# Kernel optimization log

Measured on AMD Instinct MI355X. Metric: run time of the kernel, lower is better.

## Reference

```python
import jax, jax.numpy as jnp
import numpy as np

DIM = 2048
N_HEADS = 32
N_KV_HEADS = 8
HEAD_DIM = DIM // N_HEADS  # 64
MAX_SEQ_LEN = 2048
ROPE_THETA = 10000.0
ROPE_SCALE = 1.0  # ("linear", 1.0)


def build_rope_cache(seq_len):
    # standard half-rotation RoPE cache with linear position scaling
    inv_freq = 1.0 / (ROPE_THETA ** (jnp.arange(0, HEAD_DIM, 2, dtype=jnp.float32) / HEAD_DIM))
    t = jnp.arange(seq_len, dtype=jnp.float32) / ROPE_SCALE
    freqs = jnp.outer(t, inv_freq)                      # [S, HD/2]
    emb = jnp.concatenate([freqs, freqs], axis=-1)      # [S, HD]
    return jnp.cos(emb), jnp.sin(emb)


def apply_rope(x, cos, sin):
    # x: [B, S, H, D]; cos/sin: [S, D]
    c = cos[None, :, None, :]
    s = sin[None, :, None, :]
    x1, x2 = jnp.split(x, 2, axis=-1)
    rot = jnp.concatenate([-x2, x1], axis=-1)           # rotate_half
    return x * c + rot * s


def setup_inputs() -> dict:
    key = jax.random.key(0)
    kx, kq, kk, kv, ko = jax.random.split(key, 5)
    B, S = 1, 2048
    x = jax.random.normal(kx, (B, S, DIM), dtype=jnp.float32)
    # nn.Linear weights stored [out_features, in_features]
    wq = jax.random.normal(kq, (DIM, DIM), dtype=jnp.float32) * 0.02
    wk = jax.random.normal(kk, (HEAD_DIM * N_KV_HEADS, DIM), dtype=jnp.float32) * 0.02
    wv = jax.random.normal(kv, (HEAD_DIM * N_KV_HEADS, DIM), dtype=jnp.float32) * 0.02
    wo = jax.random.normal(ko, (DIM, DIM), dtype=jnp.float32) * 0.02
    return {"x": x, "wq": wq, "wk": wk, "wv": wv, "wo": wo}


def reference(x, wq, wk, wv, wo):
    B, S, _ = x.shape
    g = N_HEADS // N_KV_HEADS  # GQA expand factor
    q = (x @ wq.T).reshape(B, S, N_HEADS, HEAD_DIM)
    k = (x @ wk.T).reshape(B, S, N_KV_HEADS, HEAD_DIM)
    v = (x @ wv.T).reshape(B, S, N_KV_HEADS, HEAD_DIM)
    cos, sin = build_rope_cache(S)
    q = apply_rope(q, cos, sin)
    k = apply_rope(k, cos, sin)
    # group q heads with their kv head instead of repeat_interleave on k/v
    q = q.transpose(0, 2, 1, 3).reshape(B, N_KV_HEADS, g, S, HEAD_DIM)
    k = k.transpose(0, 2, 1, 3)   # [B, Hkv, S, D]
    v = v.transpose(0, 2, 1, 3)
    scale = 1.0 / jnp.sqrt(jnp.asarray(HEAD_DIM, dtype=x.dtype))
    scores = jnp.einsum('bhgqd,bhkd->bhgqk', q, k) * scale  # [B,Hkv,g,S,S]
    causal = jnp.tril(jnp.ones((S, S), dtype=bool))
    scores = jnp.where(causal[None, None, None, :, :], scores, -jnp.inf)
    p = jax.nn.softmax(scores, axis=-1)
    out = jnp.einsum('bhgqk,bhkd->bhgqd', p, v)             # [B,Hkv,g,S,D]
    out = out.reshape(B, N_HEADS, S, HEAD_DIM).transpose(0, 2, 1, 3).reshape(B, S, DIM)
    return out @ wo.T
```

## Files before the change

### kernel.cpp

```cpp
#include <hip/hip_runtime.h>
#include <hip/hip_bf16.h>
#include <cstdint>
#include <cstddef>

#define DIM_ 2048
#define SLEN 2048
#define NQH 32
#define NKVH 8
#define HDIM 64
#define KVDIM 512

typedef __attribute__((ext_vector_type(8))) short short8;
typedef __attribute__((ext_vector_type(4))) float f32x4;
typedef __attribute__((ext_vector_type(16))) float f32x16;
typedef __attribute__((ext_vector_type(4))) unsigned int u32x4;

#define QSCALE 0.1803368801111243f

__device__ __forceinline__ unsigned short f2bf(float f) {
  unsigned u = __builtin_bit_cast(unsigned, f);
  u += 0x7FFFu + ((u >> 16) & 1u);
  return (unsigned short)(u >> 16);
}

__device__ __forceinline__ unsigned cvt_pk_bf16(float lo, float hi) {
  unsigned r;
  asm("v_cvt_pk_bf16_f32 %0, %1, %2" : "=v"(r) : "v"(lo), "v"(hi));
  return r;
}

__device__ __forceinline__ void gload_lds16(const void* g, void* l) {
  __builtin_amdgcn_global_load_lds(
      (const __attribute__((address_space(1))) void*)g,
      (__attribute__((address_space(3))) void*)l, 16, 0, 0);
}

__global__ void cvt_bf16_kernel(const float* __restrict__ in,
                                unsigned short* __restrict__ out, int n) {
  int i = (blockIdx.x * blockDim.x + threadIdx.x) * 8;
  if (i >= n) return;
  float4 a = *(const float4*)(in + i);
  float4 b = *(const float4*)(in + i + 4);
  ushort4 o0, o1;
  o0.x = f2bf(a.x); o0.y = f2bf(a.y); o0.z = f2bf(a.z); o0.w = f2bf(a.w);
  o1.x = f2bf(b.x); o1.y = f2bf(b.y); o1.z = f2bf(b.z); o1.w = f2bf(b.w);
  *(ushort4*)(out + i) = o0;
  *(ushort4*)(out + i + 4) = o1;
}

__global__ void rope_table_kernel(float* __restrict__ cosT, float* __restrict__ sinT) {
  int idx = blockIdx.x * blockDim.x + threadIdx.x;
  int s = idx >> 5, i = idx & 31;
  float inv = expf(-(float)i * (9.210340371976184f / 32.0f));
  float fr = (float)s * inv;
  cosT[idx] = cosf(fr);
  sinT[idx] = sinf(fr);
}

#define GSTAGE(buf, kt)                                                        \
  do {                                                                         \
    _Pragma("unroll") for (int r = 0; r < 2; ++r) {                            \
      const int L = r * 512 + tid;                                             \
      const int row = L >> 3;                                                  \
      const int scb = ((L & 7) * 16) ^ ((row & 7) << 4);                       \
      gload_lds16((const char*)A + ((size_t)(row0 + row) * DIM_ + kt) * 2 + scb, \
                  sA[buf] + (size_t)(r * 512 + wv * 64) * 8);                  \
      gload_lds16((const char*)B + ((size_t)(col0 + row) * DIM_ + kt) * 2 + scb, \
                  sB[buf] + (size_t)(r * 512 + wv * 64) * 8);                  \
    }                                                                          \
  } while (0)

#define GCOMPUTE(cur)                                                          \
  do {                                                                         \
    _Pragma("unroll") for (int ks = 0; ks < 2; ++ks) {                         \
      short8 af[2], bfr[4];                                                    \
      _Pragma("unroll") for (int m = 0; m < 2; ++m) {                          \
        const int row = wr + m * 16 + lrow;                                    \
        const int cB = (ks * 64 + lkb) ^ ((row & 7) << 4);                     \
        af[m] = *(const short8*)(sA[cur] + row * 64 + (cB >> 1));              \
      }                                                                        \
      _Pragma("unroll") for (int n = 0; n < 4; ++n) {                          \
        const int row = wc + n * 16 + lrow;                                    \
        const int cB = (ks * 64 + lkb) ^ ((row & 7) << 4);                     \
        bfr[n] = *(const short8*)(sB[cur] + row * 64 + (cB >> 1));             \
      }                                                                        \
      _Pragma("unroll") for (int m = 0; m < 2; ++m)                            \
          _Pragma("unroll") for (int n = 0; n < 4; ++n) acc[m][n] =            \
              __builtin_amdgcn_mfma_f32_16x16x32_bf16(af[m], bfr[n],           \
                                                      acc[m][n], 0, 0, 0);     \
    }                                                                          \
  } while (0)

__global__ __launch_bounds__(512, 2)
void gemm_qkv(const unsigned short* __restrict__ A,
              const unsigned short* __restrict__ B,
              unsigned short* __restrict__ Qr,
              unsigned short* __restrict__ Kr,
              unsigned short* __restrict__ Vtp,
              const float* __restrict__ cosT,
              const float* __restrict__ sinT) {
  __shared__ unsigned short sA[2][128 * 64];
  __shared__ unsigned short sB[2][128 * 64];
  const int tid = threadIdx.x;
  const int wv = tid >> 6, ln = tid & 63;
  const int row0 = blockIdx.x * 128;
  const int col0 = blockIdx.y * 128;
  const int wr = (wv >> 1) * 32, wc = (wv & 1) * 64;
  const int lrow = ln & 15, lkb = (ln >> 4) * 16;
  f32x4 acc[2][4] = {};

  GSTAGE(0, 0);
  for (int t = 0; t < 32; ++t) {
    __syncthreads();
    if (t + 1 < 32) GSTAGE((t + 1) & 1, (t + 1) * 64);
    GCOMPUTE(t & 1);
  }
  const int orow = (ln >> 4) * 4;
  const int by = blockIdx.y;
  if (by < 16) {
#pragma unroll
    for (int m = 0; m < 2; ++m)
#pragma unroll
      for (int j = 0; j < 4; ++j) {
        const int s = row0 + wr + m * 16 + orow + j;
#pragma unroll
        for (int n = 0; n < 2; ++n) {
          const int d1 = n * 16 + lrow;
          const float cv = cosT[s * 32 + d1], sv = sinT[s * 32 + d1];
          const float x1 = acc[m][n][j], x2 = acc[m][n + 2][j];
          const size_t base = (size_t)s * DIM_ + col0 + wc + d1;
          Qr[base] = f2bf((x1 * cv - x2 * sv) * QSCALE);
          Qr[base + 32] = f2bf((x2 * cv + x1 * sv) * QSCALE);
        }
      }
  } else if (by < 20) {
    const int cb = col0 - 2048;
#pragma unroll
    for (int m = 0; m < 2; ++m)
#pragma unroll
      for (int j = 0; j < 4; ++j) {
        const int s = row0 + wr + m * 16 + orow + j;
#pragma unroll
        for (int n = 0; n < 2; ++n) {
          const int d1 = n * 16 + lrow;
          const float cv = cosT[s * 32 + d1], sv = sinT[s * 32 + d1];
          const float x1 = acc[m][n][j], x2 = acc[m][n + 2][j];
          const size_t base = (size_t)s * KVDIM + cb + wc + d1;
          Kr[base] = f2bf(x1 * cv - x2 * sv);
          Kr[base + 32] = f2bf(x2 * cv + x1 * sv);
        }
      }
  } else {
    const int cb = col0 - 2560;
#pragma unroll
    for (int m = 0; m < 2; ++m)
#pragma unroll
      for (int n = 0; n < 4; ++n)
#pragma unroll
        for (int j = 0; j < 4; ++j) {
          const int s = row0 + wr + m * 16 + orow + j;
          const int vc = cb + wc + n * 16 + lrow;
          Vtp[(size_t)vc * SLEN + s] = f2bf(acc[m][n][j]);
        }
  }
}

__global__ __launch_bounds__(512, 2)
void gemm_bt_f32(const unsigned short* __restrict__ A,
                 const unsigned short* __restrict__ B, float* __restrict__ C) {
  __shared__ unsigned short sA[2][128 * 64];
  __shared__ unsigned short sB[2][128 * 64];
  const int tid = threadIdx.x;
  const int wv = tid >> 6, ln = tid & 63;
  const int row0 = blockIdx.x * 128;
  const int col0 = blockIdx.y * 128;
  const int wr = (wv >> 1) * 32, wc = (wv & 1) * 64;
  const int lrow = ln & 15, lkb = (ln >> 4) * 16;
  f32x4 acc[2][4] = {};

  GSTAGE(0, 0);
  for (int t = 0; t < 32; ++t) {
    __syncthreads();
    if (t + 1 < 32) GSTAGE((t + 1) & 1, (t + 1) * 64);
    GCOMPUTE(t & 1);
  }
  const int orow = (ln >> 4) * 4;
#pragma unroll
  for (int m = 0; m < 2; ++m)
#pragma unroll
    for (int n = 0; n < 4; ++n)
#pragma unroll
      for (int j = 0; j < 4; ++j)
        C[(size_t)(row0 + wr + m * 16 + orow + j) * DIM_ + col0 + wc + n * 16 + lrow] =
            acc[m][n][j];
}

__global__ __launch_bounds__(256, 2)
void attn4_kernel(const unsigned short* __restrict__ Q,
                  const unsigned short* __restrict__ Kc,
                  const unsigned short* __restrict__ Vt,
                  unsigned short* __restrict__ AO) {
  __shared__ __align__(16) char smem[16384];
  const int id = blockIdx.x;
  const int kvh = id & 7, hg = (id >> 3) & 3;
  const int c = 15 - (id >> 5);
  const int h = kvh * 4 + hg;
  const int tid = threadIdx.x;
  const int w = tid >> 6, l = tid & 63;
  const int l31 = l & 31, hi = l >> 5;
  const int wq0 = c * 128 + w * 32;
  const int qrow = wq0 + l31;
  const int ntw = (wq0 + 95) >> 6;

  const unsigned short* Kb = Kc + kvh * HDIM;
  const unsigned short* Vb = Vt + (size_t)kvh * HDIM * SLEN;

  short8 qf[4];
  {
    const unsigned short* qp = Q + (size_t)qrow * DIM_ + h * HDIM + hi * 8;
#pragma unroll
    for (int d = 0; d < 4; ++d) qf[d] = *(const short8*)(qp + d * 16);
  }
  f32x16 o[2] = {};
  float mrun = -1e30f, lrun = 0.f;

  auto loadK = [&](short8* kf, int t) {
    const unsigned short* kp = Kb + (size_t)(t * 64 + l31) * KVDIM + hi * 8;
#pragma unroll
    for (int d = 0; d < 4; ++d) {
      kf[d] = *(const short8*)(kp + d * 16);
      kf[4 + d] = *(const short8*)(kp + 32 * KVDIM + d * 16);
    }
  };

  auto body = [&](int t, const short8* kf) {
    const int k0 = t * 64;
    short8 vf0[4], vf1[4];
    {
      const unsigned short* vp = Vb + (size_t)l31 * SLEN + k0 + hi * 8;
#pragma unroll
      for (int d = 0; d < 4; ++d) {
        vf0[d] = *(const short8*)(vp + d * 16);
        vf1[d] = *(const short8*)(vp + (size_t)32 * SLEN + d * 16);
      }
    }
    f32x16 s0 = {}, s1 = {};
    __builtin_amdgcn_s_setprio(1);
#pragma unroll
    for (int d = 0; d < 4; ++d) {
      s0 = __builtin_amdgcn_mfma_f32_32x32x16_bf16(kf[d], qf[d], s0, 0, 0, 0);
      s1 = __builtin_amdgcn_mfma_f32_32x32x16_bf16(kf[4 + d], qf[d], s1, 0, 0, 0);
    }
    __builtin_amdgcn_s_setprio(0);

    float p[32];
#pragma unroll
    for (int r = 0; r < 16; ++r) { p[r] = s0[r]; p[16 + r] = s1[r]; }
    if (k0 + 63 > wq0) {
#pragma unroll
      for (int r = 0; r < 16; ++r) {
        const int ka = k0 + (r & 3) + 8 * (r >> 2) + 4 * hi;
        if (ka > qrow) p[r] = -1e30f;
        if (ka + 32 > qrow) p[16 + r] = -1e30f;
      }
    }
    float t16[16];
#pragma unroll
    for (int i = 0; i < 16; ++i) t16[i] = fmaxf(p[i], p[i + 16]);
#pragma unroll
    for (int i = 0; i < 8; ++i) t16[i] = fmaxf(t16[i], t16[i + 8]);
#pragma unroll
    for (int i = 0; i < 4; ++i) t16[i] = fmaxf(t16[i], t16[i + 4]);
    float pmax = fmaxf(fmaxf(t16[0], t16[1]), fmaxf(t16[2], t16[3]));
    pmax = fmaxf(pmax, __shfl_xor(pmax, 32));
    if (!__all(pmax - mrun <= 8.0f)) {
      const float mnew = fmaxf(mrun, pmax);
      const float alpha = exp2f(mrun - mnew);
      mrun = mnew;
      lrun *= alpha;
#pragma unroll
      for (int r = 0; r < 16; ++r) { o[0][r] *= alpha; o[1][r] *= alpha; }
    }
#pragma unroll
    for (int i = 0; i < 32; ++i) p[i] = exp2f(p[i] - mrun);
    float u16[16];
#pragma unroll
    for (int i = 0; i < 16; ++i) u16[i] = p[i] + p[i + 16];
#pragma unroll
    for (int i = 0; i < 8; ++i) u16[i] += u16[i + 8];
#pragma unroll
    for (int i = 0; i < 4; ++i) u16[i] += u16[i + 4];
    float rs = (u16[0] + u16[1]) + (u16[2] + u16[3]);
    rs += __shfl_xor(rs, 32);
    lrun += rs;

    unsigned pa[8], pb[8];
#pragma unroll
    for (int i = 0; i < 8; ++i) {
      pa[i] = cvt_pk_bf16(p[i * 4 + 0], p[i * 4 + 1]);
      pb[i] = cvt_pk_bf16(p[i * 4 + 2], p[i * 4 + 3]);
    }
    __builtin_amdgcn_s_setprio(1);
#pragma unroll
    for (int kb = 0; kb < 4; ++kb) {
      const int i0 = (kb >> 1) * 4 + (kb & 1) * 2;
      const int i1 = i0 + 1;
      unsigned w0 = pa[i0], w2 = pa[i1];
      asm("v_permlane32_swap_b32 %0, %1" : "+v"(w0), "+v"(w2));
      unsigned w1 = pb[i0], w3 = pb[i1];
      asm("v_permlane32_swap_b32 %0, %1" : "+v"(w1), "+v"(w3));
      u32x4 uu = {w0, w1, w2, w3};
      short8 pf = __builtin_bit_cast(short8, uu);
      o[0] = __builtin_amdgcn_mfma_f32_32x32x16_bf16(vf0[kb], pf, o[0], 0, 0, 0);
      o[1] = __builtin_amdgcn_mfma_f32_32x32x16_bf16(vf1[kb], pf, o[1], 0, 0, 0);
    }
    __builtin_amdgcn_s_setprio(0);
  };

  short8 ka[8], kb_[8];
  loadK(ka, 0);
  int t = 0;
  for (;;) {
    if (t + 1 < ntw) loadK(kb_, t + 1);
    body(t, ka);
    if (++t >= ntw) break;
    if (t + 1 < ntw) loadK(ka, t + 1);
    body(t, kb_);
    if (++t >= ntw) break;
  }

  const float inv = 1.0f / lrun;
  char* tw = smem + w * 4096;
#pragma unroll
  for (int db = 0; db < 2; ++db)
#pragma unroll
    for (int g = 0; g < 4; ++g) {
      ushort4 v;
      v.x = f2bf(o[db][g * 4 + 0] * inv);
      v.y = f2bf(o[db][g * 4 + 1] * inv);
      v.z = f2bf(o[db][g * 4 + 2] * inv);
      v.w = f2bf(o[db][g * 4 + 3] * inv);
      const int d0 = db * 32 + g * 8 + hi * 4;
      *(ushort4*)(tw + l31 * 128 + ((d0 * 2) ^ ((l31 & 7) << 4))) = v;
    }
  {
    const int rr = l >> 1, cc = (l & 1) * 32;
    unsigned short* ap = AO + (size_t)(c * 128 + w * 32 + rr) * DIM_ + h * HDIM + cc;
#pragma unroll
    for (int pq = 0; pq < 4; ++pq) {
      const int colb = ((cc + pq * 8) * 2) ^ ((rr & 7) << 4);
      short8 v = *(const short8*)(tw + rr * 128 + colb);
      *(short8*)(ap + pq * 8) = v;
    }
  }
}

extern "C" void kernel_launch(void* const* d_in, const int* in_sizes, int n_in,
                              void* d_out, int out_size, void* d_ws, size_t ws_size,
                              hipStream_t stream) {
  const float* x  = (const float*)d_in[0];
  const float* wq = (const float*)d_in[1];
  const float* wk = (const float*)d_in[2];
  const float* wv = (const float*)d_in[3];
  const float* wo = (const float*)d_in[4];
  float* out = (float*)d_out;
  char* ws = (char*)d_ws;
  const size_t MB = 1u << 20;
  unsigned short* bx   = (unsigned short*)(ws + 0 * MB);
  unsigned short* bqkv = (unsigned short*)(ws + 8 * MB);
  unsigned short* bwo  = (unsigned short*)(ws + 20 * MB);
  unsigned short* Qr   = (unsigned short*)(ws + 28 * MB);
  unsigned short* Kr   = (unsigned short*)(ws + 36 * MB);
  unsigned short* Vt   = (unsigned short*)(ws + 38 * MB);
  unsigned short* AO   = (unsigned short*)(ws + 40 * MB);
  float* cosT = (float*)(ws + 48 * MB);
  float* sinT = (float*)(ws + 48 * MB + 256 * 1024);

  rope_table_kernel<<<SLEN * 32 / 256, 256, 0, stream>>>(cosT, sinT);
  cvt_bf16_kernel<<<(2048 * 2048 / 8) / 256, 256, 0, stream>>>(x, bx, 2048 * 2048);
  cvt_bf16_kernel<<<(2048 * 2048 / 8) / 256, 256, 0, stream>>>(wq, bqkv, 2048 * 2048);
  cvt_bf16_kernel<<<(512 * 2048 / 8) / 256, 256, 0, stream>>>(wk, bqkv + 2048 * 2048, 512 * 2048);
  cvt_bf16_kernel<<<(512 * 2048 / 8) / 256, 256, 0, stream>>>(wv, bqkv + 2560 * 2048, 512 * 2048);
  cvt_bf16_kernel<<<(2048 * 2048 / 8) / 256, 256, 0, stream>>>(wo, bwo, 2048 * 2048);

  gemm_qkv<<<dim3(16, 24), 512, 0, stream>>>(bx, bqkv, Qr, Kr, Vt, cosT, sinT);

  attn4_kernel<<<512, 256, 0, stream>>>(Qr, Kr, Vt, AO);

  gemm_bt_f32<<<dim3(16, 16), 512, 0, stream>>>(AO, bwo, out);
}
```

Measured before the change: 262.1 us.

## Restructure attention as single-wave blocks staging K/V via async LDS loads

Replaces the 4-wave attention kernel with 2048 single-wave blocks, each handling 32 query rows of one head. K and V tiles are now staged into shared memory with direct global-to-LDS loads, and the next tile's load is overlapped with compute through explicit vmcnt/lgkmcnt waits. The upper half of the diagonal tile is skipped when it is fully masked. The aim is better load balance, latency hiding and less wasted causal work. In exchange, K/V are no longer shared across waves of a block, so more global and L2 traffic per block, and the hand-written wait counts are fragile.

```diff
diff --git a/kernel.cpp b/kernel.cpp
--- a/kernel.cpp
+++ b/kernel.cpp
@@ -195,25 +195,44 @@
             acc[m][n][j];
 }
 
-__global__ __launch_bounds__(256, 2)
-void attn4_kernel(const unsigned short* __restrict__ Q,
+#define WAITV8() asm volatile("s_waitcnt vmcnt(8)" ::: "memory")
+#define WAITV0() asm volatile("s_waitcnt vmcnt(0)" ::: "memory")
+#define WAITL0() asm volatile("s_waitcnt lgkmcnt(0)" ::: "memory")
+
+__global__ __launch_bounds__(64, 2)
+void attn5_kernel(const unsigned short* __restrict__ Q,
                   const unsigned short* __restrict__ Kc,
                   const unsigned short* __restrict__ Vt,
                   unsigned short* __restrict__ AO) {
   __shared__ __align__(16) char smem[16384];
   const int id = blockIdx.x;
-  const int kvh = id & 7, hg = (id >> 3) & 3;
-  const int c = 15 - (id >> 5);
-  const int h = kvh * 4 + hg;
-  const int tid = threadIdx.x;
-  const int w = tid >> 6, l = tid & 63;
+  const int h = id & 31;
+  const int c = 63 - (id >> 5);
+  const int kvh = h >> 2;
+  const int l = threadIdx.x;
   const int l31 = l & 31, hi = l >> 5;
-  const int wq0 = c * 128 + w * 32;
+  const int wq0 = c * 32;
   const int qrow = wq0 + l31;
-  const int ntw = (wq0 + 95) >> 6;
-
-  const unsigned short* Kb = Kc + kvh * HDIM;
-  const unsigned short* Vb = Vt + (size_t)kvh * HDIM * SLEN;
+  const int nt = (c + 2) >> 1;
+
+  const char* Kb = (const char*)(Kc + kvh * HDIM);
+  const char* Vb = (const char*)(Vt + (size_t)kvh * HDIM * SLEN);
+
+  const int lrow8 = l >> 3;
+  const int scb = ((l & 7) * 16) ^ (lrow8 << 4);
+
+  auto stageK = [&](int t) {
+#pragma unroll
+    for (int i = 0; i < 8; ++i)
+      gload_lds16(Kb + (size_t)(t * 64 + i * 8 + lrow8) * (KVDIM * 2) + scb,
+                  smem + i * 1024);
+  };
+  auto stageV = [&](int t) {
+#pragma unroll
+    for (int i = 0; i < 8; ++i)
+      gload_lds16(Vb + (size_t)(i * 8 + lrow8) * (SLEN * 2) + t * 128 + scb,
+                  smem + 8192 + i * 1024);
+  };
 
   short8 qf[4];
   {
@@ -224,32 +243,35 @@
   f32x16 o[2] = {};
   float mrun = -1e30f, lrun = 0.f;
 
-  auto loadK = [&](short8* kf, int t) {
-    const unsigned short* kp = Kb + (size_t)(t * 64 + l31) * KVDIM + hi * 8;
+  stageK(0);
+  stageV(0);
+
+  for (int t = 0; t < nt; ++t) {
+    const int k0 = t * 64;
+    const bool last = (t + 1 >= nt);
+    const bool skipHi = (k0 >= wq0);
+
+    WAITV8();
+    short8 kfr[8];
 #pragma unroll
     for (int d = 0; d < 4; ++d) {
-      kf[d] = *(const short8*)(kp + d * 16);
-      kf[4 + d] = *(const short8*)(kp + 32 * KVDIM + d * 16);
-    }
-  };
-
-  auto body = [&](int t, const short8* kf) {
-    const int k0 = t * 64;
-    short8 vf0[4], vf1[4];
-    {
-      const unsigned short* vp = Vb + (size_t)l31 * SLEN + k0 + hi * 8;
-#pragma unroll
-      for (int d = 0; d < 4; ++d) {
-        vf0[d] = *(const short8*)(vp + d * 16);
-        vf1[d] = *(const short8*)(vp + (size_t)32 * SLEN + d * 16);
-      }
-    }
+      const int colb = (d * 32 + hi * 16) ^ ((l31 & 7) << 4);
+      kfr[d] = *(const short8*)(smem + l31 * 128 + colb);
+      kfr[4 + d] = *(const short8*)(smem + (32 + l31) * 128 + colb);
+    }
+    WAITL0();
+    __builtin_amdgcn_sched_barrier(0);
+    if (!last) stageK(t + 1);
+
     f32x16 s0 = {}, s1 = {};
     __builtin_amdgcn_s_setprio(1);
 #pragma unroll
-    for (int d = 0; d < 4; ++d) {
-      s0 = __builtin_amdgcn_mfma_f32_32x32x16_bf16(kf[d], qf[d], s0, 0, 0, 0);
-      s1 = __builtin_amdgcn_mfma_f32_32x32x16_bf16(kf[4 + d], qf[d], s1, 0, 0, 0);
+    for (int d = 0; d < 4; ++d)
+      s0 = __builtin_amdgcn_mfma_f32_32x32x16_bf16(kfr[d], qf[d], s0, 0, 0, 0);
+    if (!skipHi) {
+#pragma unroll
+      for (int d = 0; d < 4; ++d)
+        s1 = __builtin_amdgcn_mfma_f32_32x32x16_bf16(kfr[4 + d], qf[d], s1, 0, 0, 0);
     }
     __builtin_amdgcn_s_setprio(0);
 
@@ -261,7 +283,7 @@
       for (int r = 0; r < 16; ++r) {
         const int ka = k0 + (r & 3) + 8 * (r >> 2) + 4 * hi;
         if (ka > qrow) p[r] = -1e30f;
-        if (ka + 32 > qrow) p[16 + r] = -1e30f;
+        if (skipHi || ka + 32 > qrow) p[16 + r] = -1e30f;
       }
     }
     float t16[16];
@@ -300,9 +322,23 @@
       pa[i] = cvt_pk_bf16(p[i * 4 + 0], p[i * 4 + 1]);
       pb[i] = cvt_pk_bf16(p[i * 4 + 2], p[i * 4 + 3]);
     }
+
+    if (!last) { WAITV8(); } else { WAITV0(); }
+    short8 vfr[8];
+#pragma unroll
+    for (int kb = 0; kb < 4; ++kb) {
+      const int colb = (kb * 32 + hi * 16) ^ ((l31 & 7) << 4);
+      vfr[kb] = *(const short8*)(smem + 8192 + l31 * 128 + colb);
+      vfr[4 + kb] = *(const short8*)(smem + 8192 + (32 + l31) * 128 + colb);
+    }
+    WAITL0();
+    __builtin_amdgcn_sched_barrier(0);
+    if (!last) stageV(t + 1);
+
     __builtin_amdgcn_s_setprio(1);
 #pragma unroll
     for (int kb = 0; kb < 4; ++kb) {
+      if (skipHi && kb >= 2) break;
       const int i0 = (kb >> 1) * 4 + (kb & 1) * 2;
       const int i1 = i0 + 1;
       unsigned w0 = pa[i0], w2 = pa[i1];
@@ -311,26 +347,13 @@
       asm("v_permlane32_swap_b32 %0, %1" : "+v"(w1), "+v"(w3));
       u32x4 uu = {w0, w1, w2, w3};
       short8 pf = __builtin_bit_cast(short8, uu);
-      o[0] = __builtin_amdgcn_mfma_f32_32x32x16_bf16(vf0[kb], pf, o[0], 0, 0, 0);
-      o[1] = __builtin_amdgcn_mfma_f32_32x32x16_bf16(vf1[kb], pf, o[1], 0, 0, 0);
+      o[0] = __builtin_amdgcn_mfma_f32_32x32x16_bf16(vfr[kb], pf, o[0], 0, 0, 0);
+      o[1] = __builtin_amdgcn_mfma_f32_32x32x16_bf16(vfr[4 + kb], pf, o[1], 0, 0, 0);
     }
     __builtin_amdgcn_s_setprio(0);
-  };
-
-  short8 ka[8], kb_[8];
-  loadK(ka, 0);
-  int t = 0;
-  for (;;) {
-    if (t + 1 < ntw) loadK(kb_, t + 1);
-    body(t, ka);
-    if (++t >= ntw) break;
-    if (t + 1 < ntw) loadK(ka, t + 1);
-    body(t, kb_);
-    if (++t >= ntw) break;
   }
 
   const float inv = 1.0f / lrun;
-  char* tw = smem + w * 4096;
 #pragma unroll
   for (int db = 0; db < 2; ++db)
 #pragma unroll
@@ -341,15 +364,15 @@
       v.z = f2bf(o[db][g * 4 + 2] * inv);
       v.w = f2bf(o[db][g * 4 + 3] * inv);
       const int d0 = db * 32 + g * 8 + hi * 4;
-      *(ushort4*)(tw + l31 * 128 + ((d0 * 2) ^ ((l31 & 7) << 4))) = v;
+      *(ushort4*)(smem + l31 * 128 + ((d0 * 2) ^ ((l31 & 7) << 4))) = v;
     }
   {
-    const int rr = l >> 1, cc = (l & 1) * 32;
-    unsigned short* ap = AO + (size_t)(c * 128 + w * 32 + rr) * DIM_ + h * HDIM + cc;
+    const int rr = l >> 1, cc2 = (l & 1) * 32;
+    unsigned short* ap = AO + (size_t)(wq0 + rr) * DIM_ + h * HDIM + cc2;
 #pragma unroll
     for (int pq = 0; pq < 4; ++pq) {
-      const int colb = ((cc + pq * 8) * 2) ^ ((rr & 7) << 4);
-      short8 v = *(const short8*)(tw + rr * 128 + colb);
+      const int colb = ((cc2 + pq * 8) * 2) ^ ((rr & 7) << 4);
+      short8 v = *(const short8*)(smem + rr * 128 + colb);
       *(short8*)(ap + pq * 8) = v;
     }
   }
@@ -385,7 +408,7 @@
 
   gemm_qkv<<<dim3(16, 24), 512, 0, stream>>>(bx, bqkv, Qr, Kr, Vt, cosT, sinT);
 
-  attn4_kernel<<<512, 256, 0, stream>>>(Qr, Kr, Vt, AO);
+  attn5_kernel<<<2048, 64, 0, stream>>>(Qr, Kr, Vt, AO);
 
   gemm_bt_f32<<<dim3(16, 16), 512, 0, stream>>>(AO, bwo, out);
 }
```

Measured after the change: 223.2 us. 1.17x faster.
